# Kernel tuning notes

Measured on AMD Instinct MI355X. Metric: run time of the kernel, lower is better.

The kernel has to match this reference:

```python
import jax, jax.numpy as jnp
import numpy as np

HEADS = 4
NEG_SLOPE = 0.2
LN_EPS = 1e-5


def _layernorm(h, g, b):
    mu = h.mean(-1, keepdims=True)
    var = ((h - mu) ** 2).mean(-1, keepdims=True)
    return (h - mu) / jnp.sqrt(var + LN_EPS) * g + b


def _forward(x, edge_attr, vnf_context,
             w_node, b_node, w_edge_emb, b_edge_emb,
             w_eproj, b_eproj, w_vnf, b_vnf,
             attn_w1, attn_b1, attn_w2, attn_b2, attn_w3, attn_b3,
             gat_w, gat_att_src, gat_att_dst, gat_we, gat_att_e, gat_b,
             ln_g, ln_b,
             venc_w1, venc_b1, venc_w2, venc_b2,
             lstm_wih, lstm_whh, lstm_bih, lstm_bhh,
             out_w1, out_b1, out_w2, out_b2, out_w3, out_b3,
             edge_index):
    N = x.shape[0]
    C = w_node.shape[1]  # hidden_dim = per-head out_channels
    L = gat_w.shape[0]
    src, dst = edge_index[0], edge_index[1]

    # embeddings
    xh = x @ w_node + b_node                        # [N, C]
    ea = edge_attr @ w_edge_emb + b_edge_emb        # [E, C]

    # EdgeAttentionLayer (vnf_context branch, no network_state)
    ef = ea @ w_eproj + b_eproj                     # [E, C]
    vemb = vnf_context @ w_vnf + b_vnf              # [C]
    comb = jnp.concatenate([ef, jnp.broadcast_to(vemb, ef.shape)], axis=-1)
    h1 = jax.nn.relu(comb @ attn_w1 + attn_b1)
    h2 = jax.nn.relu(h1 @ attn_w2 + attn_b2)
    edge_attention = jax.nn.sigmoid(h2 @ attn_w3 + attn_b3)[:, 0]   # [E]
    e_enh = ef * edge_attention[:, None]            # weighted edge features [E, C]

    # PathQualityAwareConv stack: GATConv(heads=4, concat=False, edge_dim=C)
    for l in range(L):
        xr = xh
        xs = (xh @ gat_w[l]).reshape(N, HEADS, C)               # [N, H, C]
        efeat = (e_enh @ gat_we[l]).reshape(-1, HEADS, C)        # [E, H, C]
        a = (jnp.einsum('ehc,hc->eh', xs[src], gat_att_src[l])
             + jnp.einsum('ehc,hc->eh', xs[dst], gat_att_dst[l])
             + jnp.einsum('ehc,hc->eh', efeat, gat_att_e[l]))
        a = jax.nn.leaky_relu(a, NEG_SLOPE)
        amax = jax.ops.segment_max(a, dst, num_segments=N)
        amax = jnp.where(jnp.isfinite(amax), amax, 0.0)
        ae = jnp.exp(a - amax[dst])
        denom = jax.ops.segment_sum(ae, dst, num_segments=N)
        alpha = ae / (denom[dst] + 1e-16)                        # [E, H]
        msg = xs[src] * alpha[:, :, None]                        # [E, H, C]
        agg = jax.ops.segment_sum(msg, dst, num_segments=N)      # [N, H, C]
        h = agg.mean(axis=1) + gat_b[l]                          # concat=False -> head mean
        h = _layernorm(h, ln_g[l], ln_b[l])
        xh = h + xr                                              # residual (same size)

    # vnf context encoder
    v = jax.nn.relu(vnf_context @ venc_w1 + venc_b1) @ venc_w2 + venc_b2  # [C]

    # Set2Set pooling, single graph, processing_steps=3, LSTM(2C -> C)
    hS = jnp.zeros((C,), xh.dtype)
    cS = jnp.zeros((C,), xh.dtype)
    q_star = jnp.zeros((2 * C,), xh.dtype)
    for _ in range(3):
        gates = lstm_wih @ q_star + lstm_bih + lstm_whh @ hS + lstm_bhh
        gi, gf, gg, go = jnp.split(gates, 4)
        cS = jax.nn.sigmoid(gf) * cS + jax.nn.sigmoid(gi) * jnp.tanh(gg)
        hS = jax.nn.sigmoid(go) * jnp.tanh(cS)
        q = hS
        a_sc = jax.nn.softmax(xh @ q)                            # [N]
        r = a_sc @ xh                                            # [C]
        q_star = jnp.concatenate([q, r])

    combined = jnp.concatenate([q_star, v])                      # [3C]
    o = jax.nn.relu(combined @ out_w1 + out_b1)
    o = jax.nn.relu(o @ out_w2 + out_b2)
    o = jax.nn.relu(o @ out_w3 + out_b3)
    return o[None, :]                                            # [1, output_dim]


def setup_inputs() -> dict:
    key = jax.random.key(0)
    ks = jax.random.split(key, 40)
    N, E, C, L = 50000, 200000, 128, 3
    H = HEADS
    rn = lambda k, s, sc=0.05: (jax.random.normal(k, s, jnp.float32) * sc)
    z = lambda *s: jnp.zeros(s, jnp.float32)
    return {
        'x': jax.random.normal(ks[0], (N, 8), jnp.float32),
        'edge_index': jax.random.randint(ks[1], (2, E), 0, N),
        'edge_attr': jax.random.uniform(ks[2], (E, 4), dtype=jnp.float32),
        'vnf_context': jax.random.normal(ks[3], (6,), jnp.float32),
        'w_node': rn(ks[4], (8, C)), 'b_node': z(C),
        'w_edge_emb': rn(ks[5], (4, C)), 'b_edge_emb': z(C),
        'w_eproj': rn(ks[6], (C, C)), 'b_eproj': z(C),
        'w_vnf': rn(ks[7], (6, C)), 'b_vnf': z(C),
        'attn_w1': rn(ks[8], (2 * C, C)), 'attn_b1': z(C),
        'attn_w2': rn(ks[9], (C, C // 2)), 'attn_b2': z(C // 2),
        'attn_w3': rn(ks[10], (C // 2, 1)), 'attn_b3': z(1),
        'gat_w': rn(ks[11], (L, C, H * C)),
        'gat_att_src': rn(ks[12], (L, H, C)),
        'gat_att_dst': rn(ks[13], (L, H, C)),
        'gat_we': rn(ks[14], (L, C, H * C)),
        'gat_att_e': rn(ks[15], (L, H, C)),
        'gat_b': z(L, C),
        'ln_g': jnp.ones((L, C), jnp.float32), 'ln_b': z(L, C),
        'venc_w1': rn(ks[16], (6, C)), 'venc_b1': z(C),
        'venc_w2': rn(ks[17], (C, C)), 'venc_b2': z(C),
        'lstm_wih': rn(ks[18], (4 * C, 2 * C)), 'lstm_whh': rn(ks[19], (4 * C, C)),
        'lstm_bih': z(4 * C), 'lstm_bhh': z(4 * C),
        'out_w1': rn(ks[20], (3 * C, C)), 'out_b1': z(C),
        'out_w2': rn(ks[21], (C, C // 2)), 'out_b2': z(C // 2),
        'out_w3': rn(ks[22], (C // 2, 256)), 'out_b3': z(256),
    }


def reference(x, edge_index, edge_attr, vnf_context,
              w_node, b_node, w_edge_emb, b_edge_emb,
              w_eproj, b_eproj, w_vnf, b_vnf,
              attn_w1, attn_b1, attn_w2, attn_b2, attn_w3, attn_b3,
              gat_w, gat_att_src, gat_att_dst, gat_we, gat_att_e, gat_b,
              ln_g, ln_b,
              venc_w1, venc_b1, venc_w2, venc_b2,
              lstm_wih, lstm_whh, lstm_bih, lstm_bhh,
              out_w1, out_b1, out_w2, out_b2, out_w3, out_b3):
    return _forward(x, edge_attr, vnf_context,
                    w_node, b_node, w_edge_emb, b_edge_emb,
                    w_eproj, b_eproj, w_vnf, b_vnf,
                    attn_w1, attn_b1, attn_w2, attn_b2, attn_w3, attn_b3,
                    gat_w, gat_att_src, gat_att_dst, gat_we, gat_att_e, gat_b,
                    ln_g, ln_b,
                    venc_w1, venc_b1, venc_w2, venc_b2,
                    lstm_wih, lstm_whh, lstm_bih, lstm_bhh,
                    out_w1, out_b1, out_w2, out_b2, out_w3, out_b3,
                    edge_index)
```

## Files before the change

kernel.cpp:

```cpp
#include <hip/hip_runtime.h>
#include <math.h>

#define CC 128
#define HH 4
#define LL 3
#define LNEPS 1e-5f

typedef unsigned int u32;
typedef unsigned short ushort;
typedef float f32x16 __attribute__((ext_vector_type(16)));
typedef __bf16 bf16x8 __attribute__((ext_vector_type(8)));
union Frag { uint4 q; bf16x8 b; };

__device__ __forceinline__ u32 fenc(float f){ u32 u=__float_as_uint(f); return (u&0x80000000u)? ~u : (u|0x80000000u); }
__device__ __forceinline__ float fdec(u32 u){ return (u&0x80000000u)? __uint_as_float(u&0x7FFFFFFFu) : __uint_as_float(~u); }
__device__ __forceinline__ ushort bf16rne(float x){ u32 u=__float_as_uint(x); return (ushort)((u + 0x7FFF + ((u>>16)&1))>>16); }
__device__ __forceinline__ float bf2f(ushort h){ return __uint_as_float(((u32)h)<<16); }


__global__ void k_att_collapse(const float* __restrict__ W, const float* __restrict__ att, float* __restrict__ out){
  int idx = blockIdx.x*blockDim.x + threadIdx.x;
  if(idx >= LL*CC*HH) return;
  int h = idx % HH; int k = (idx/HH)%CC; int l = idx/(HH*CC);
  const float* w = W + ((size_t)(l*CC+k))*(HH*CC) + h*CC;
  const float* a = att + (size_t)(l*HH+h)*CC;
  float s=0.f;
  for(int c=0;c<CC;c++) s += w[c]*a[c];
  out[idx] = s;
}

__global__ void k_We(const float* __restrict__ w_ee, const float* __restrict__ w_ep, float* __restrict__ We){
  int idx = blockIdx.x*blockDim.x + threadIdx.x;
  if(idx >= 4*CC) return;
  int c = idx & (CC-1); int k = idx >> 7;
  float s=0.f;
  for(int m=0;m<CC;m++) s += w_ee[k*CC+m]*w_ep[m*CC+c];
  We[idx]=s;
}

__global__ void k_be_vemb(const float* __restrict__ b_ee, const float* __restrict__ w_ep, const float* __restrict__ b_ep,
                          const float* __restrict__ vnf, const float* __restrict__ w_vnf, const float* __restrict__ b_vnf,
                          float* __restrict__ be, float* __restrict__ vemb){
  int t = threadIdx.x;
  if(t<CC){
    float s=b_ep[t];
    for(int m=0;m<CC;m++) s += b_ee[m]*w_ep[m*CC+t];
    be[t]=s;
  } else if(t<2*CC){
    int c=t-CC;
    float s=b_vnf[c];
    for(int j=0;j<6;j++) s += vnf[j]*w_vnf[j*CC+c];
    vemb[c]=s;
  }
}

__global__ void k_h1eff(const float* __restrict__ We, const float* __restrict__ be, const float* __restrict__ vemb,
                        const float* __restrict__ w1, const float* __restrict__ b1,
                        float* __restrict__ Wh1, float* __restrict__ bh1){
  int idx = blockIdx.x*blockDim.x + threadIdx.x;
  if(idx < 4*CC){
    int c = idx & (CC-1); int k = idx>>7;
    float s=0.f;
    for(int m=0;m<CC;m++) s += We[k*CC+m]*w1[m*CC+c];
    Wh1[idx]=s;
  } else if(idx < 5*CC){
    int c = idx - 4*CC;
    float s=b1[c];
    for(int m=0;m<CC;m++) s += be[m]*w1[m*CC+c];
    for(int j=0;j<CC;j++) s += vemb[j]*w1[(CC+j)*CC+c];
    bh1[c]=s;
  }
}

__global__ void k_aelin(const float* __restrict__ We, const float* __restrict__ be, const float* __restrict__ wattE,
                        float* __restrict__ aelin, float* __restrict__ aebias){
  int t = threadIdx.x;
  if(t<48){
    int l=t>>4, k=(t>>2)&3, h=t&3;
    float s=0.f;
    for(int m=0;m<CC;m++) s += We[k*CC+m]*wattE[(size_t)(l*CC+m)*HH+h];
    aelin[t]=s;
  } else if(t<60){
    int i=t-48; int l=i>>2, h=i&3;
    float s=0.f;
    for(int m=0;m<CC;m++) s += be[m]*wattE[(size_t)(l*CC+m)*HH+h];
    aebias[i]=s;
  }
}

__global__ void k_wsplit(const float* __restrict__ gat_w, ushort* __restrict__ BHT, ushort* __restrict__ BLT){
  int idx = blockIdx.x*blockDim.x + threadIdx.x;
  if(idx >= LL*512*CC) return;
  int l = idx >> 16;
  int r = idx & 65535;
  int hk = r >> 7;
  int c  = r & 127;
  int k = hk & 127, h = hk >> 7;
  float v = gat_w[((size_t)(l*CC + k))*(HH*CC) + h*CC + c] * 0.25f;
  ushort hi = bf16rne(v);
  ushort lo = bf16rne(v - bf2f(hi));
  size_t pos = (size_t)l*65536 + ((size_t)(c>>5)*64 + (hk>>3))*256 + (size_t)((c&31)*8 + (hk&7));
  BHT[pos]=hi; BLT[pos]=lo;
}

__global__ void k_vvec(const float* __restrict__ vnf, const float* __restrict__ w1, const float* __restrict__ b1,
                       const float* __restrict__ w2, const float* __restrict__ b2, float* __restrict__ v){
  __shared__ float hv[CC];
  int t=threadIdx.x;
  float s=b1[t];
  for(int j=0;j<6;j++) s += vnf[j]*w1[j*CC+t];
  hv[t]=fmaxf(s,0.f);
  __syncthreads();
  float o=b2[t];
  for(int j=0;j<CC;j++) o += hv[j]*w2[j*CC+t];
  v[t]=o;
}

__global__ void k_node_embed(const float* __restrict__ x, const float* __restrict__ w, const float* __restrict__ b,
                             float* __restrict__ xh, int N){
  int idx=blockIdx.x*blockDim.x+threadIdx.x;
  if(idx>=N*CC) return;
  int c=idx&(CC-1); int n=idx>>7;
  const float* xr = x+(size_t)n*8;
  float s=b[c];
  #pragma unroll
  for(int k=0;k<8;k++) s += xr[k]*w[k*CC+c];
  xh[idx]=s;
}

__global__ void k_count(const int* __restrict__ dst, int* __restrict__ counts, int E){
  int e=blockIdx.x*blockDim.x+threadIdx.x;
  if(e<E) atomicAdd(&counts[dst[e]],1);
}

__global__ __launch_bounds__(256) void k_scan_blk(const int* __restrict__ counts, int* __restrict__ offsets,
                                                  int* __restrict__ bsum, int N){
  __shared__ int sv[256];
  int t=threadIdx.x; int i=blockIdx.x*256+t;
  int v = (i<N)? counts[i] : 0;
  sv[t]=v;
  __syncthreads();
  for(int off=1;off<256;off<<=1){
    int add = (t>=off)? sv[t-off]:0;
    __syncthreads();
    sv[t]+=add;
    __syncthreads();
  }
  if(i<N) offsets[i]=sv[t]-v;
  if(t==255) bsum[blockIdx.x]=sv[255];
}

__global__ __launch_bounds__(1024) void k_scan_top(int* __restrict__ bsum, int nb){
  __shared__ int sv[1024];
  int t=threadIdx.x;
  int v = (t<nb)? bsum[t] : 0;
  sv[t]=v;
  __syncthreads();
  for(int off=1;off<1024;off<<=1){
    int add = (t>=off)? sv[t-off]:0;
    __syncthreads();
    sv[t]+=add;
    __syncthreads();
  }
  if(t<nb) bsum[t]=sv[t]-v;
}

__global__ void k_scan_add(int* __restrict__ offsets, const int* __restrict__ bsum, int N, int E){
  int i=blockIdx.x*blockDim.x+threadIdx.x;
  if(i<N) offsets[i]+=bsum[i>>8];
  if(i==0) offsets[N]=E;
}

__global__ void k_fill(const int* __restrict__ dst, const int* __restrict__ offsets, int* __restrict__ cursor,
                       int* __restrict__ elist, int E){
  int e=blockIdx.x*blockDim.x+threadIdx.x;
  if(e<E){ int d=dst[e]; int pos=atomicAdd(&cursor[d],1); elist[offsets[d]+pos]=e; }
}

__global__ __launch_bounds__(256) void k_edge_attn(
    const float* __restrict__ edge_attr,
    const float* __restrict__ Wh1, const float* __restrict__ bh1,
    const float* __restrict__ attn_w2, const float* __restrict__ attn_b2,
    const float* __restrict__ attn_w3, const float* __restrict__ attn_b3,
    const float* __restrict__ aelin, const float* __restrict__ aebias,
    float* __restrict__ a_e, int E)
{
  __shared__ float s_w2[CC*64];
  __shared__ float s_h1t[64*64];
  __shared__ float s_eat[4*64];
  __shared__ float s_wh1t[CC*4];
  __shared__ float s_bh1[CC];
  __shared__ float s_b2[64];
  __shared__ float s_w3[64];
  __shared__ float s_lin[48];
  __shared__ float s_lbias[12];
  int t = threadIdx.x;
  for(int i=t;i<CC*64;i+=256) s_w2[i]=attn_w2[i];
  for(int i=t;i<CC*4;i+=256){ int c=i>>2, k=i&3; s_wh1t[i]=Wh1[k*CC+c]; }
  if(t<CC) s_bh1[t]=bh1[t];
  else if(t<CC+64) s_b2[t-CC]=attn_b2[t-CC];
  else if(t<CC+128) s_w3[t-CC-64]=attn_w3[t-CC-64];
  if(t<48) s_lin[t]=aelin[t];
  else if(t<60) s_lbias[t-48]=aebias[t-48];
  float b3v = attn_b3[0];
  int e0 = blockIdx.x*64;
  if(t<64){
    int e=e0+t;
    float4 v = (e<E)? *(const float4*)&edge_attr[(size_t)e*4] : make_float4(0.f,0.f,0.f,0.f);
    s_eat[t]=v.x; s_eat[64+t]=v.y; s_eat[128+t]=v.z; s_eat[192+t]=v.w;
  }
  int eg=t>>4, og=t&15;
  float acc[4][4];
  #pragma unroll
  for(int i=0;i<4;i++){ acc[i][0]=0.f; acc[i][1]=0.f; acc[i][2]=0.f; acc[i][3]=0.f; }
  for(int half=0;half<2;half++){
    __syncthreads();
    for(int i=t;i<64*64;i+=256){
      int kl=i>>6, e=i&63, k=half*64+kl;
      float4 w = *(const float4*)&s_wh1t[k*4];
      float v = s_bh1[k] + s_eat[e]*w.x + s_eat[64+e]*w.y + s_eat[128+e]*w.z + s_eat[192+e]*w.w;
      s_h1t[i] = fmaxf(v,0.f);
    }
    __syncthreads();
    const float* w2h = s_w2 + half*4096;
    #pragma unroll 8
    for(int k=0;k<64;k++){
      float4 a = *(const float4*)&s_h1t[k*64 + eg*4];
      float4 b = *(const float4*)&w2h[k*64 + og*4];
      acc[0][0]+=a.x*b.x; acc[0][1]+=a.x*b.y; acc[0][2]+=a.x*b.z; acc[0][3]+=a.x*b.w;
      acc[1][0]+=a.y*b.x; acc[1][1]+=a.y*b.y; acc[1][2]+=a.y*b.z; acc[1][3]+=a.y*b.w;
      acc[2][0]+=a.z*b.x; acc[2][1]+=a.z*b.y; acc[2][2]+=a.z*b.z; acc[2][3]+=a.z*b.w;
      acc[3][0]+=a.w*b.x; acc[3][1]+=a.w*b.y; acc[3][2]+=a.w*b.z; acc[3][3]+=a.w*b.w;
    }
  }
  float4 b2v = *(const float4*)&s_b2[og*4];
  float4 w3v = *(const float4*)&s_w3[og*4];
  float att[4];
  #pragma unroll
  for(int i=0;i<4;i++){
    float p = fmaxf(acc[i][0]+b2v.x,0.f)*w3v.x + fmaxf(acc[i][1]+b2v.y,0.f)*w3v.y
            + fmaxf(acc[i][2]+b2v.z,0.f)*w3v.z + fmaxf(acc[i][3]+b2v.w,0.f)*w3v.w;
    #pragma unroll
    for(int off=1;off<16;off<<=1) p += __shfl_xor(p,off);
    att[i] = 1.f/(1.f+expf(-(p+b3v)));
  }
  if(og<12){
    int l=og>>2, h=og&3;
    float w0=s_lin[l*16+h], w1=s_lin[l*16+4+h], w2x=s_lin[l*16+8+h], w3x=s_lin[l*16+12+h];
    float lb=s_lbias[l*4+h];
    #pragma unroll
    for(int i=0;i<4;i++){
      int el=eg*4+i; int e=e0+el;
      if(e<E){
        float v = s_eat[el]*w0 + s_eat[64+el]*w1 + s_eat[128+el]*w2x + s_eat[192+el]*w3x + lb;
        a_e[((size_t)l*E+e)*4+h] = att[i]*v;
      }
    }
  }
}

__global__ void k_node_ad(const float* __restrict__ xh, const float* __restrict__ wS, const float* __restrict__ wD,
                          float* __restrict__ asrc, float* __restrict__ adst, int N){
  int idx = blockIdx.x*blockDim.x + threadIdx.x;
  if(idx >= N*8) return;
  int o = idx & 7; int n = idx >> 3;
  const float* w = ((o<4)? wS : wD) + (o&3);
  const float* xr = xh + (size_t)n*CC;
  float s=0.f;
  for(int k=0;k<CC;k++) s += xr[k]*w[(size_t)k*HH];
  ((o<4)? asrc : adst)[n*4+(o&3)] = s;
}

__global__ __launch_bounds__(256) void k_aggregate(
    const float* __restrict__ xh, const int* __restrict__ srcArr,
    const float* __restrict__ aeL, const float* __restrict__ asrc, const float* __restrict__ adst,
    const int* __restrict__ offsets, const int* __restrict__ elist,
    ushort* __restrict__ sH, ushort* __restrict__ sL, int N)
{
  int wave = threadIdx.x>>6, lane = threadIdx.x&63;
  int n = blockIdx.x*4+wave;
  if(n>=N) return;
  int beg = offsets[n];
  int deg = offsets[n+1]-beg;
  const float4* ae4 = (const float4*)aeL;
  const float4* as4 = (const float4*)asrc;
  float4 ad = ((const float4*)adst)[n];
  float mx0=-1e30f,mx1=-1e30f,mx2=-1e30f,mx3=-1e30f;
  for(int base=0;base<deg;base+=64){
    int i=base+lane;
    if(i<deg){
      int e = elist[beg+i];
      float4 ae = ae4[e];
      float4 as = as4[srcArr[e]];
      float a0=as.x+ad.x+ae.x; a0=(a0>0.f)?a0:0.2f*a0;
      float a1=as.y+ad.y+ae.y; a1=(a1>0.f)?a1:0.2f*a1;
      float a2=as.z+ad.z+ae.z; a2=(a2>0.f)?a2:0.2f*a2;
      float a3=as.w+ad.w+ae.w; a3=(a3>0.f)?a3:0.2f*a3;
      mx0=fmaxf(mx0,a0); mx1=fmaxf(mx1,a1); mx2=fmaxf(mx2,a2); mx3=fmaxf(mx3,a3);
    }
  }
  #pragma unroll
  for(int o=32;o>=1;o>>=1){
    mx0=fmaxf(mx0,__shfl_xor(mx0,o));
    mx1=fmaxf(mx1,__shfl_xor(mx1,o));
    mx2=fmaxf(mx2,__shfl_xor(mx2,o));
    mx3=fmaxf(mx3,__shfl_xor(mx3,o));
  }
  float sm0=0,sm1=0,sm2=0,sm3=0;
  float acc0=0,acc1=0,acc2=0,acc3=0,acc4=0,acc5=0,acc6=0,acc7=0;
  for(int base=0;base<deg;base+=64){
    int i=base+lane;
    float ex0=0,ex1=0,ex2=0,ex3=0; int mysrc=0;
    if(i<deg){
      int e = elist[beg+i];
      mysrc = srcArr[e];
      float4 ae = ae4[e];
      float4 as = as4[mysrc];
      float a0=as.x+ad.x+ae.x; a0=(a0>0.f)?a0:0.2f*a0;
      float a1=as.y+ad.y+ae.y; a1=(a1>0.f)?a1:0.2f*a1;
      float a2=as.z+ad.z+ae.z; a2=(a2>0.f)?a2:0.2f*a2;
      float a3=as.w+ad.w+ae.w; a3=(a3>0.f)?a3:0.2f*a3;
      ex0=expf(a0-mx0); ex1=expf(a1-mx1); ex2=expf(a2-mx2); ex3=expf(a3-mx3);
      sm0+=ex0; sm1+=ex1; sm2+=ex2; sm3+=ex3;
    }
    int cnt = deg-base; if(cnt>64) cnt=64;
    for(int j=0;j<cnt;j++){
      int sr = __shfl(mysrc,j);
      float al0=__shfl(ex0,j), al1=__shfl(ex1,j), al2=__shfl(ex2,j), al3=__shfl(ex3,j);
      const float* xr = xh + (size_t)sr*CC;
      float x0 = xr[lane], x1 = xr[lane+64];
      acc0 += al0*x0; acc1 += al0*x1;
      acc2 += al1*x0; acc3 += al1*x1;
      acc4 += al2*x0; acc5 += al2*x1;
      acc6 += al3*x0; acc7 += al3*x1;
    }
  }
  #pragma unroll
  for(int o=32;o>=1;o>>=1){
    sm0+=__shfl_xor(sm0,o); sm1+=__shfl_xor(sm1,o); sm2+=__shfl_xor(sm2,o); sm3+=__shfl_xor(sm3,o);
  }
  float i0=1.f/(sm0+1e-16f), i1=1.f/(sm1+1e-16f), i2=1.f/(sm2+1e-16f), i3=1.f/(sm3+1e-16f);
  size_t rowbase = ((size_t)(n>>5))*64*256 + (size_t)((n&31)*8);
  auto put=[&](int hk, float v){
    ushort hi = bf16rne(v);
    ushort lo = bf16rne(v - bf2f(hi));
    size_t pos = rowbase + (size_t)(hk>>3)*256 + (hk&7);
    sH[pos]=hi; sL[pos]=lo;
  };
  put(lane, acc0*i0);      put(lane+64, acc1*i0);
  put(128+lane, acc2*i1);  put(128+lane+64, acc3*i1);
  put(256+lane, acc4*i2);  put(256+lane+64, acc5*i2);
  put(384+lane, acc6*i3);  put(384+lane+64, acc7*i3);
}

__global__ __launch_bounds__(128) void k_gemm_ln_mfma(
    const ushort* __restrict__ AH, const ushort* __restrict__ AL,
    const ushort* __restrict__ BH, const ushort* __restrict__ BL,
    const float* __restrict__ bias, const float* __restrict__ lng, const float* __restrict__ lnb,
    float* __restrict__ xh, int N)
{
  int tid = threadIdx.x;
  int w = tid>>6, lane = tid&63;
  int rlane = lane&31, khalf = lane>>5;
  int rb0 = blockIdx.x*4 + w*2;
  f32x16 acc[2][4];
  #pragma unroll
  for(int b=0;b<2;b++)
    #pragma unroll
    for(int t=0;t<4;t++)
      #pragma unroll
      for(int j=0;j<16;j++) acc[b][t][j]=0.f;

  const size_t laneoff = (size_t)(rlane*8);
  for(int ks=0; ks<32; ++ks){
    int kq = ks*2 + khalf;
    Frag ah[2], al[2];
    #pragma unroll
    for(int b=0;b<2;b++){
      size_t base = (((size_t)(rb0+b)*64 + kq)<<8) + laneoff;
      ah[b].q = *(const uint4*)(AH + base);
      al[b].q = *(const uint4*)(AL + base);
    }
    #pragma unroll
    for(int t=0;t<4;t++){
      size_t bb = (((size_t)t*64 + kq)<<8) + laneoff;
      Frag bh, bl;
      bh.q = *(const uint4*)(BH + bb);
      bl.q = *(const uint4*)(BL + bb);
      #pragma unroll
      for(int b=0;b<2;b++){
        acc[b][t] = __builtin_amdgcn_mfma_f32_32x32x16_bf16(ah[b].b, bh.b, acc[b][t], 0,0,0);
        acc[b][t] = __builtin_amdgcn_mfma_f32_32x32x16_bf16(ah[b].b, bl.b, acc[b][t], 0,0,0);
        acc[b][t] = __builtin_amdgcn_mfma_f32_32x32x16_bf16(al[b].b, bh.b, acc[b][t], 0,0,0);
      }
    }
  }
  float bias4[4], g4[4], eb4[4];
  #pragma unroll
  for(int t=0;t<4;t++){ int c=t*32+rlane; bias4[t]=bias[c]; g4[t]=lng[c]; eb4[t]=lnb[c]; }
  #pragma unroll
  for(int b=0;b<2;b++){
    #pragma unroll
    for(int reg=0; reg<16; ++reg){
      int rloc = (reg&3) + 8*(reg>>2) + 4*khalf;
      int grow = (rb0+b)*32 + rloc;
      float x0=acc[b][0][reg]+bias4[0];
      float x1=acc[b][1][reg]+bias4[1];
      float x2=acc[b][2][reg]+bias4[2];
      float x3=acc[b][3][reg]+bias4[3];
      float s = x0+x1+x2+x3;
      #pragma unroll
      for(int off=1; off<32; off<<=1) s += __shfl_xor(s, off);
      float mu = s*(1.f/CC);
      x0-=mu; x1-=mu; x2-=mu; x3-=mu;
      float q = x0*x0+x1*x1+x2*x2+x3*x3;
      #pragma unroll
      for(int off=1; off<32; off<<=1) q += __shfl_xor(q, off);
      float inv = rsqrtf(q*(1.f/CC)+LNEPS);
      if(grow < N){
        size_t gi = (size_t)grow*CC + rlane;
        xh[gi+ 0]  = x0*inv*g4[0] + eb4[0] + xh[gi+ 0];
        xh[gi+32]  = x1*inv*g4[1] + eb4[1] + xh[gi+32];
        xh[gi+64]  = x2*inv*g4[2] + eb4[2] + xh[gi+64];
        xh[gi+96]  = x3*inv*g4[3] + eb4[3] + xh[gi+96];
      }
    }
  }
}

__global__ __launch_bounds__(512) void k_lstm(const float* __restrict__ wih, const float* __restrict__ whh,
                    const float* __restrict__ bih, const float* __restrict__ bhh,
                    const float* __restrict__ qstar, float* __restrict__ hS, float* __restrict__ cS){
  __shared__ float sq[2*CC];
  __shared__ float sh[CC];
  __shared__ float sg[4*CC];
  int t=threadIdx.x;
  if(t<2*CC) sq[t]=qstar[t];
  else if(t<3*CC) sh[t-2*CC]=hS[t-2*CC];
  __syncthreads();
  float a=bih[t]+bhh[t];
  const float* wr = wih + (size_t)t*2*CC;
  for(int j=0;j<2*CC;j++) a += wr[j]*sq[j];
  const float* hr = whh + (size_t)t*CC;
  for(int j=0;j<CC;j++) a += hr[j]*sh[j];
  sg[t]=a;
  __syncthreads();
  if(t<CC){
    float gi=sg[t], gf=sg[CC+t], gg=sg[2*CC+t], go=sg[3*CC+t];
    float c = 1.f/(1.f+expf(-gf))*cS[t] + 1.f/(1.f+expf(-gi))*tanhf(gg);
    float h = 1.f/(1.f+expf(-go))*tanhf(c);
    cS[t]=c; hS[t]=h;
  }
}

__global__ __launch_bounds__(256) void k_scores(const float* __restrict__ xh, const float* __restrict__ q,
                                                float* __restrict__ sc, u32* __restrict__ scmax, int N){
  int t=threadIdx.x; int wave=t>>6, lane=t&63;
  float q0=q[lane], q1=q[lane+64];
  float wmax=-1e30f;
  for(int n=blockIdx.x*4+wave; n<N; n+=gridDim.x*4){
    const float* xr = xh+(size_t)n*CC;
    float v = xr[lane]*q0 + xr[lane+64]*q1;
    #pragma unroll
    for(int o=32;o>=1;o>>=1) v += __shfl_xor(v,o);
    if(lane==0) sc[n]=v;
    wmax = fmaxf(wmax,v);
  }
  __shared__ float sm[4];
  if(lane==0) sm[wave]=wmax;
  __syncthreads();
  if(t==0){
    float m = fmaxf(fmaxf(sm[0],sm[1]),fmaxf(sm[2],sm[3]));
    atomicMax(scmax, fenc(m));
  }
}

__global__ __launch_bounds__(256) void k_r(const float* __restrict__ xh, const float* __restrict__ sc,
                                           const u32* __restrict__ scmax, float* __restrict__ r,
                                           float* __restrict__ total, int N){
  int t=threadIdx.x; int c = t&(CC-1); int half = t>>7;
  float mx = fdec(*scmax);
  float acc=0.f, et=0.f;
  for(int n=blockIdx.x*2+half; n<N; n+=gridDim.x*2){
    float e = expf(sc[n]-mx);
    acc += e*xh[(size_t)n*CC+c];
    et += (c==0)? e : 0.f;
  }
  __shared__ float sacc[256];
  __shared__ float set_[2];
  sacc[t]=acc;
  if(c==0) set_[half]=et;
  __syncthreads();
  if(t<CC) atomicAdd(&r[t], sacc[t]+sacc[t+CC]);
  if(t==0) atomicAdd(total, set_[0]+set_[1]);
}

__global__ void k_finalize(const float* __restrict__ hS, const float* __restrict__ r,
                           const float* __restrict__ total, float* __restrict__ qstar){
  int t=threadIdx.x;
  if(t<CC) qstar[t]=hS[t];
  else if(t<2*CC) qstar[t]=r[t-CC]/total[0];
}

__global__ __launch_bounds__(256) void k_out(
  const float* __restrict__ qstar, const float* __restrict__ vvec,
  const float* __restrict__ w1, const float* __restrict__ b1,
  const float* __restrict__ w2, const float* __restrict__ b2,
  const float* __restrict__ w3, const float* __restrict__ b3, float* __restrict__ out)
{
  __shared__ float comb[3*CC];
  __shared__ float o1[CC];
  __shared__ float o2[64];
  int t=threadIdx.x;
  if(t<2*CC) comb[t]=qstar[t];
  if(t<CC) comb[2*CC+t]=vvec[t];
  __syncthreads();
  if(t<CC){
    float a=b1[t];
    for(int j=0;j<3*CC;j++) a += comb[j]*w1[j*CC+t];
    o1[t]=fmaxf(a,0.f);
  }
  __syncthreads();
  if(t<64){
    float a=b2[t];
    for(int j=0;j<CC;j++) a += o1[j]*w2[j*64+t];
    o2[t]=fmaxf(a,0.f);
  }
  __syncthreads();
  {
    float a=b3[t];
    for(int j=0;j<64;j++) a += o2[j]*w3[j*256+t];
    out[t]=fmaxf(a,0.f);
  }
}

extern "C" void kernel_launch(void* const* d_in, const int* in_sizes, int n_in,
                              void* d_out, int out_size, void* d_ws, size_t ws_size,
                              hipStream_t stream){
  (void)n_in; (void)out_size; (void)ws_size;
  const float* x        = (const float*)d_in[0];
  const int*   eidx     = (const int*)  d_in[1];
  const float* edge_attr= (const float*)d_in[2];
  const float* vnf      = (const float*)d_in[3];
  const float* w_node   = (const float*)d_in[4];
  const float* b_node   = (const float*)d_in[5];
  const float* w_ee     = (const float*)d_in[6];
  const float* b_ee     = (const float*)d_in[7];
  const float* w_ep     = (const float*)d_in[8];
  const float* b_ep     = (const float*)d_in[9];
  const float* w_vnf    = (const float*)d_in[10];
  const float* b_vnf    = (const float*)d_in[11];
  const float* attn_w1  = (const float*)d_in[12];
  const float* attn_b1  = (const float*)d_in[13];
  const float* attn_w2  = (const float*)d_in[14];
  const float* attn_b2  = (const float*)d_in[15];
  const float* attn_w3  = (const float*)d_in[16];
  const float* attn_b3  = (const float*)d_in[17];
  const float* gat_w    = (const float*)d_in[18];
  const float* att_src  = (const float*)d_in[19];
  const float* att_dst  = (const float*)d_in[20];
  const float* gat_we   = (const float*)d_in[21];
  const float* att_e    = (const float*)d_in[22];
  const float* gat_b    = (const float*)d_in[23];
  const float* ln_g     = (const float*)d_in[24];
  const float* ln_b     = (const float*)d_in[25];
  const float* venc_w1  = (const float*)d_in[26];
  const float* venc_b1  = (const float*)d_in[27];
  const float* venc_w2  = (const float*)d_in[28];
  const float* venc_b2  = (const float*)d_in[29];
  const float* lstm_wih = (const float*)d_in[30];
  const float* lstm_whh = (const float*)d_in[31];
  const float* lstm_bih = (const float*)d_in[32];
  const float* lstm_bhh = (const float*)d_in[33];
  const float* out_w1   = (const float*)d_in[34];
  const float* out_b1   = (const float*)d_in[35];
  const float* out_w2   = (const float*)d_in[36];
  const float* out_b2   = (const float*)d_in[37];
  const float* out_w3   = (const float*)d_in[38];
  const float* out_b3   = (const float*)d_in[39];

  const int N = in_sizes[0]/8;
  const int E = in_sizes[1]/2;
  const int* srcA = eidx;
  const int* dstA = eidx + E;

  const int Npad = ((N+127)/128)*128;
  const size_t atile = (size_t)(Npad/32)*64*256;
  const int nb = (N+255)/256;

  char* wp = (char*)d_ws;
  auto alloc = [&](size_t bytes)->void*{ void* p=(void*)wp; wp += (bytes+255)&~(size_t)255; return p; };
  float* xh    = (float*)alloc((size_t)N*CC*4);
  ushort* sbufH= (ushort*)alloc(atile*2);
  ushort* sbufL= (ushort*)alloc(atile*2);
  ushort* BHT  = (ushort*)alloc((size_t)LL*512*CC*2);
  ushort* BLT  = (ushort*)alloc((size_t)LL*512*CC*2);
  float* a_e   = (float*)alloc((size_t)LL*E*HH*4);
  float* asrc  = (float*)alloc((size_t)N*HH*4);
  float* adst  = (float*)alloc((size_t)N*HH*4);
  int* counts  = (int*)alloc((size_t)N*4);
  int* offsets = (int*)alloc((size_t)(N+1)*4);
  int* cursor  = (int*)alloc((size_t)N*4);
  int* elist   = (int*)alloc((size_t)E*4);
  int* bsum    = (int*)alloc((size_t)nb*4);
  float* sc    = (float*)alloc((size_t)N*4);
  float* wattS = (float*)alloc((size_t)LL*CC*HH*4);
  float* wattD = (float*)alloc((size_t)LL*CC*HH*4);
  float* wattE = (float*)alloc((size_t)LL*CC*HH*4);
  float* We    = (float*)alloc(4*CC*4);
  float* be    = (float*)alloc(CC*4);
  float* vemb  = (float*)alloc(CC*4);
  float* Wh1   = (float*)alloc(4*CC*4);
  float* bh1   = (float*)alloc(CC*4);
  float* aelin = (float*)alloc(48*4);
  float* aebias= (float*)alloc(12*4);
  float* vvec  = (float*)alloc(CC*4);
  float* lbuf  = (float*)alloc(4*CC*4);
  float* hS=lbuf; float* cS=lbuf+CC; float* qstar=lbuf+2*CC;
  float* s2s   = (float*)alloc(130*4);

  k_att_collapse<<<6,256,0,stream>>>(gat_w, att_src, wattS);
  k_att_collapse<<<6,256,0,stream>>>(gat_w, att_dst, wattD);
  k_att_collapse<<<6,256,0,stream>>>(gat_we, att_e, wattE);
  k_We<<<2,256,0,stream>>>(w_ee, w_ep, We);
  k_be_vemb<<<1,256,0,stream>>>(b_ee, w_ep, b_ep, vnf, w_vnf, b_vnf, be, vemb);
  k_h1eff<<<3,256,0,stream>>>(We, be, vemb, attn_w1, attn_b1, Wh1, bh1);
  k_aelin<<<1,64,0,stream>>>(We, be, wattE, aelin, aebias);
  k_wsplit<<<(LL*512*CC+255)/256,256,0,stream>>>(gat_w, BHT, BLT);
  k_vvec<<<1,CC,0,stream>>>(vnf, venc_w1, venc_b1, venc_w2, venc_b2, vvec);
  k_node_embed<<<(N*CC+255)/256,256,0,stream>>>(x, w_node, b_node, xh, N);

  hipMemsetAsync(counts, 0, (size_t)N*4, stream);
  k_count<<<(E+255)/256,256,0,stream>>>(dstA, counts, E);
  k_scan_blk<<<nb,256,0,stream>>>(counts, offsets, bsum, N);
  k_scan_top<<<1,1024,0,stream>>>(bsum, nb);
  k_scan_add<<<nb,256,0,stream>>>(offsets, bsum, N, E);
  hipMemsetAsync(cursor, 0, (size_t)N*4, stream);
  k_fill<<<(E+255)/256,256,0,stream>>>(dstA, offsets, cursor, elist, E);

  k_edge_attn<<<(E+63)/64,256,0,stream>>>(edge_attr, Wh1, bh1, attn_w2, attn_b2, attn_w3, attn_b3, aelin, aebias, a_e, E);

  for(int l=0;l<LL;l++){
    k_node_ad<<<(N*8+255)/256,256,0,stream>>>(xh, wattS+(size_t)l*CC*HH, wattD+(size_t)l*CC*HH, asrc, adst, N);
    k_aggregate<<<(N+3)/4,256,0,stream>>>(xh, srcA, a_e+(size_t)l*E*HH, asrc, adst, offsets, elist, sbufH, sbufL, N);
    k_gemm_ln_mfma<<<Npad/128,128,0,stream>>>(sbufH, sbufL,
                                              BHT+(size_t)l*512*CC, BLT+(size_t)l*512*CC,
                                              gat_b+(size_t)l*CC, ln_g+(size_t)l*CC, ln_b+(size_t)l*CC, xh, N);
  }

  hipMemsetAsync(lbuf, 0, 4*CC*4, stream);
  for(int it=0; it<3; ++it){
    k_lstm<<<1,512,0,stream>>>(lstm_wih, lstm_whh, lstm_bih, lstm_bhh, qstar, hS, cS);
    hipMemsetAsync(s2s, 0, 130*4, stream);
    k_scores<<<512,256,0,stream>>>(xh, hS, sc, (u32*)s2s, N);
    k_r<<<512,256,0,stream>>>(xh, sc, (u32*)s2s, s2s+2, s2s+1, N);
    k_finalize<<<1,256,0,stream>>>(hS, s2s+2, s2s+1, qstar);
  }

  k_out<<<1,256,0,stream>>>(qstar, vvec, out_w1, out_b1, out_w2, out_b2, out_w3, out_b3, (float*)d_out);
}
```

Before: 836.8 us.

## Restructure GAT softmax, node projections, GEMM tiling and Set2Set pooling kernels

Splits the per-node edge softmax into a separate per-(node,head) alpha kernel that writes normalized weights in place, and simplifies aggregation to a single pass with float2 loads and packed bf16 stores. It also tiles k_node_ad through shared memory and halves the per-wave row blocks in the MFMA GEMM so more blocks launch. Set2Set pooling becomes a single-pass online-softmax kernel with per-block partials plus a small reduce, dropping the memsets, atomics and score buffer. Edge-attention stages W2 in halves to cut shared memory. The alpha kernel walks edges serially per thread, which may be slow for high-degree nodes.

```diff
diff --git a/kernel.cpp b/kernel.cpp
--- a/kernel.cpp
+++ b/kernel.cpp
@@ -12,8 +12,6 @@
 typedef __bf16 bf16x8 __attribute__((ext_vector_type(8)));
 union Frag { uint4 q; bf16x8 b; };
 
-__device__ __forceinline__ u32 fenc(float f){ u32 u=__float_as_uint(f); return (u&0x80000000u)? ~u : (u|0x80000000u); }
-__device__ __forceinline__ float fdec(u32 u){ return (u&0x80000000u)? __uint_as_float(u&0x7FFFFFFFu) : __uint_as_float(~u); }
 __device__ __forceinline__ ushort bf16rne(float x){ u32 u=__float_as_uint(x); return (ushort)((u + 0x7FFF + ((u>>16)&1))>>16); }
 __device__ __forceinline__ float bf2f(ushort h){ return __uint_as_float(((u32)h)<<16); }
 
@@ -185,7 +183,7 @@
     const float* __restrict__ aelin, const float* __restrict__ aebias,
     float* __restrict__ a_e, int E)
 {
-  __shared__ float s_w2[CC*64];
+  __shared__ float s_w2[64*64];
   __shared__ float s_h1t[64*64];
   __shared__ float s_eat[4*64];
   __shared__ float s_wh1t[CC*4];
@@ -195,7 +193,6 @@
   __shared__ float s_lin[48];
   __shared__ float s_lbias[12];
   int t = threadIdx.x;
-  for(int i=t;i<CC*64;i+=256) s_w2[i]=attn_w2[i];
   for(int i=t;i<CC*4;i+=256){ int c=i>>2, k=i&3; s_wh1t[i]=Wh1[k*CC+c]; }
   if(t<CC) s_bh1[t]=bh1[t];
   else if(t<CC+64) s_b2[t-CC]=attn_b2[t-CC];
@@ -221,12 +218,12 @@
       float v = s_bh1[k] + s_eat[e]*w.x + s_eat[64+e]*w.y + s_eat[128+e]*w.z + s_eat[192+e]*w.w;
       s_h1t[i] = fmaxf(v,0.f);
     }
+    for(int i=t;i<64*64;i+=256) s_w2[i] = attn_w2[half*4096 + i];
     __syncthreads();
-    const float* w2h = s_w2 + half*4096;
     #pragma unroll 8
     for(int k=0;k<64;k++){
       float4 a = *(const float4*)&s_h1t[k*64 + eg*4];
-      float4 b = *(const float4*)&w2h[k*64 + og*4];
+      float4 b = *(const float4*)&s_w2[k*64 + og*4];
       acc[0][0]+=a.x*b.x; acc[0][1]+=a.x*b.y; acc[0][2]+=a.x*b.z; acc[0][3]+=a.x*b.w;
       acc[1][0]+=a.y*b.x; acc[1][1]+=a.y*b.y; acc[1][2]+=a.y*b.z; acc[1][3]+=a.y*b.w;
       acc[2][0]+=a.z*b.x; acc[2][1]+=a.z*b.y; acc[2][2]+=a.z*b.z; acc[2][3]+=a.z*b.w;
@@ -259,98 +256,92 @@
   }
 }
 
-__global__ void k_node_ad(const float* __restrict__ xh, const float* __restrict__ wS, const float* __restrict__ wD,
+__global__ __launch_bounds__(256) void k_node_ad(const float* __restrict__ xh, const float* __restrict__ wS, const float* __restrict__ wD,
                           float* __restrict__ asrc, float* __restrict__ adst, int N){
+  __shared__ float sx[32*129];
+  __shared__ float sw[CC*8];
+  int t = threadIdx.x;
+  int n0 = blockIdx.x*32;
+  for(int i=t;i<512;i+=256){ int k=i>>2, h=i&3; sw[k*8+h]=wS[i]; sw[k*8+4+h]=wD[i]; }
+  int lim = (N-n0 < 32 ? N-n0 : 32)*128;
+  for(int i=t;i<lim;i+=256){ int nl=i>>7, k=i&127; sx[nl*129+k] = xh[(size_t)n0*128 + i]; }
+  __syncthreads();
+  int node = t>>3, o = t&7;
+  if(n0+node < N){
+    const float* xr = sx + node*129;
+    float s=0.f;
+    #pragma unroll 8
+    for(int k=0;k<CC;k++) s += xr[k]*sw[k*8+o];
+    ((o<4)? asrc : adst)[(n0+node)*4 + (o&3)] = s;
+  }
+}
+
+__global__ void k_alpha(const float* __restrict__ asrc, const float* __restrict__ adst,
+                        const int* __restrict__ offsets, const int* __restrict__ elist,
+                        const int* __restrict__ srcArr, float* __restrict__ ael, int N){
   int idx = blockIdx.x*blockDim.x + threadIdx.x;
-  if(idx >= N*8) return;
-  int o = idx & 7; int n = idx >> 3;
-  const float* w = ((o<4)? wS : wD) + (o&3);
-  const float* xr = xh + (size_t)n*CC;
+  if(idx >= N*4) return;
+  int n = idx>>2, h = idx&3;
+  int beg = offsets[n], end = offsets[n+1];
+  if(beg==end) return;
+  float ad = adst[n*4+h];
+  float m = -1e30f;
+  for(int i=beg;i<end;i++){
+    int e = elist[i];
+    float a = asrc[srcArr[e]*4+h] + ad + ael[e*4+h];
+    a = (a>0.f)? a : 0.2f*a;
+    m = fmaxf(m,a);
+  }
   float s=0.f;
-  for(int k=0;k<CC;k++) s += xr[k]*w[(size_t)k*HH];
-  ((o<4)? asrc : adst)[n*4+(o&3)] = s;
+  for(int i=beg;i<end;i++){
+    int e = elist[i];
+    float a = asrc[srcArr[e]*4+h] + ad + ael[e*4+h];
+    a = (a>0.f)? a : 0.2f*a;
+    float ex = expf(a-m);
+    s += ex;
+    ael[e*4+h] = ex;
+  }
+  float inv = 1.f/(s+1e-16f);
+  for(int i=beg;i<end;i++){
+    int e = elist[i];
+    ael[e*4+h] *= inv;
+  }
 }
 
 __global__ __launch_bounds__(256) void k_aggregate(
     const float* __restrict__ xh, const int* __restrict__ srcArr,
-    const float* __restrict__ aeL, const float* __restrict__ asrc, const float* __restrict__ adst,
-    const int* __restrict__ offsets, const int* __restrict__ elist,
+    const float* __restrict__ alpha, const int* __restrict__ offsets, const int* __restrict__ elist,
     ushort* __restrict__ sH, ushort* __restrict__ sL, int N)
 {
   int wave = threadIdx.x>>6, lane = threadIdx.x&63;
   int n = blockIdx.x*4+wave;
   if(n>=N) return;
-  int beg = offsets[n];
-  int deg = offsets[n+1]-beg;
-  const float4* ae4 = (const float4*)aeL;
-  const float4* as4 = (const float4*)asrc;
-  float4 ad = ((const float4*)adst)[n];
-  float mx0=-1e30f,mx1=-1e30f,mx2=-1e30f,mx3=-1e30f;
-  for(int base=0;base<deg;base+=64){
-    int i=base+lane;
-    if(i<deg){
-      int e = elist[beg+i];
-      float4 ae = ae4[e];
-      float4 as = as4[srcArr[e]];
-      float a0=as.x+ad.x+ae.x; a0=(a0>0.f)?a0:0.2f*a0;
-      float a1=as.y+ad.y+ae.y; a1=(a1>0.f)?a1:0.2f*a1;
-      float a2=as.z+ad.z+ae.z; a2=(a2>0.f)?a2:0.2f*a2;
-      float a3=as.w+ad.w+ae.w; a3=(a3>0.f)?a3:0.2f*a3;
-      mx0=fmaxf(mx0,a0); mx1=fmaxf(mx1,a1); mx2=fmaxf(mx2,a2); mx3=fmaxf(mx3,a3);
-    }
-  }
-  #pragma unroll
-  for(int o=32;o>=1;o>>=1){
-    mx0=fmaxf(mx0,__shfl_xor(mx0,o));
-    mx1=fmaxf(mx1,__shfl_xor(mx1,o));
-    mx2=fmaxf(mx2,__shfl_xor(mx2,o));
-    mx3=fmaxf(mx3,__shfl_xor(mx3,o));
-  }
-  float sm0=0,sm1=0,sm2=0,sm3=0;
-  float acc0=0,acc1=0,acc2=0,acc3=0,acc4=0,acc5=0,acc6=0,acc7=0;
-  for(int base=0;base<deg;base+=64){
-    int i=base+lane;
-    float ex0=0,ex1=0,ex2=0,ex3=0; int mysrc=0;
-    if(i<deg){
-      int e = elist[beg+i];
-      mysrc = srcArr[e];
-      float4 ae = ae4[e];
-      float4 as = as4[mysrc];
-      float a0=as.x+ad.x+ae.x; a0=(a0>0.f)?a0:0.2f*a0;
-      float a1=as.y+ad.y+ae.y; a1=(a1>0.f)?a1:0.2f*a1;
-      float a2=as.z+ad.z+ae.z; a2=(a2>0.f)?a2:0.2f*a2;
-      float a3=as.w+ad.w+ae.w; a3=(a3>0.f)?a3:0.2f*a3;
-      ex0=expf(a0-mx0); ex1=expf(a1-mx1); ex2=expf(a2-mx2); ex3=expf(a3-mx3);
-      sm0+=ex0; sm1+=ex1; sm2+=ex2; sm3+=ex3;
-    }
-    int cnt = deg-base; if(cnt>64) cnt=64;
-    for(int j=0;j<cnt;j++){
-      int sr = __shfl(mysrc,j);
-      float al0=__shfl(ex0,j), al1=__shfl(ex1,j), al2=__shfl(ex2,j), al3=__shfl(ex3,j);
-      const float* xr = xh + (size_t)sr*CC;
-      float x0 = xr[lane], x1 = xr[lane+64];
-      acc0 += al0*x0; acc1 += al0*x1;
-      acc2 += al1*x0; acc3 += al1*x1;
-      acc4 += al2*x0; acc5 += al2*x1;
-      acc6 += al3*x0; acc7 += al3*x1;
-    }
-  }
-  #pragma unroll
-  for(int o=32;o>=1;o>>=1){
-    sm0+=__shfl_xor(sm0,o); sm1+=__shfl_xor(sm1,o); sm2+=__shfl_xor(sm2,o); sm3+=__shfl_xor(sm3,o);
-  }
-  float i0=1.f/(sm0+1e-16f), i1=1.f/(sm1+1e-16f), i2=1.f/(sm2+1e-16f), i3=1.f/(sm3+1e-16f);
-  size_t rowbase = ((size_t)(n>>5))*64*256 + (size_t)((n&31)*8);
-  auto put=[&](int hk, float v){
-    ushort hi = bf16rne(v);
-    ushort lo = bf16rne(v - bf2f(hi));
+  int beg = offsets[n], end = offsets[n+1];
+  const float4* al4 = (const float4*)alpha;
+  float2 ac[4];
+  #pragma unroll
+  for(int h=0;h<4;h++){ ac[h].x=0.f; ac[h].y=0.f; }
+  for(int i=beg;i<end;i++){
+    int e = elist[i];
+    int sr = srcArr[e];
+    float4 a = al4[e];
+    float2 x = *(const float2*)&xh[(size_t)sr*CC + lane*2];
+    ac[0].x += a.x*x.x; ac[0].y += a.x*x.y;
+    ac[1].x += a.y*x.x; ac[1].y += a.y*x.y;
+    ac[2].x += a.z*x.x; ac[2].y += a.z*x.y;
+    ac[3].x += a.w*x.x; ac[3].y += a.w*x.y;
+  }
+  size_t rowbase = ((size_t)(n>>5))*16384 + (size_t)((n&31)*8);
+  #pragma unroll
+  for(int h=0;h<4;h++){
+    ushort h0 = bf16rne(ac[h].x), h1 = bf16rne(ac[h].y);
+    u32 hi = (u32)h0 | ((u32)h1<<16);
+    u32 lo = (u32)bf16rne(ac[h].x - bf2f(h0)) | ((u32)bf16rne(ac[h].y - bf2f(h1))<<16);
+    int hk = h*CC + lane*2;
     size_t pos = rowbase + (size_t)(hk>>3)*256 + (hk&7);
-    sH[pos]=hi; sL[pos]=lo;
-  };
-  put(lane, acc0*i0);      put(lane+64, acc1*i0);
-  put(128+lane, acc2*i1);  put(128+lane+64, acc3*i1);
-  put(256+lane, acc4*i2);  put(256+lane+64, acc5*i2);
-  put(384+lane, acc6*i3);  put(384+lane+64, acc7*i3);
+    *(u32*)&sH[pos] = hi;
+    *(u32*)&sL[pos] = lo;
+  }
 }
 
 __global__ __launch_bounds__(128) void k_gemm_ln_mfma(
@@ -362,68 +353,57 @@
   int tid = threadIdx.x;
   int w = tid>>6, lane = tid&63;
   int rlane = lane&31, khalf = lane>>5;
-  int rb0 = blockIdx.x*4 + w*2;
-  f32x16 acc[2][4];
-  #pragma unroll
-  for(int b=0;b<2;b++)
+  int rb = blockIdx.x*2 + w;
+  f32x16 acc[4];
+  #pragma unroll
+  for(int t=0;t<4;t++)
     #pragma unroll
-    for(int t=0;t<4;t++)
-      #pragma unroll
-      for(int j=0;j<16;j++) acc[b][t][j]=0.f;
+    for(int j=0;j<16;j++) acc[t][j]=0.f;
 
   const size_t laneoff = (size_t)(rlane*8);
   for(int ks=0; ks<32; ++ks){
     int kq = ks*2 + khalf;
-    Frag ah[2], al[2];
-    #pragma unroll
-    for(int b=0;b<2;b++){
-      size_t base = (((size_t)(rb0+b)*64 + kq)<<8) + laneoff;
-      ah[b].q = *(const uint4*)(AH + base);
-      al[b].q = *(const uint4*)(AL + base);
-    }
+    size_t base = (((size_t)rb*64 + kq)<<8) + laneoff;
+    Frag ah, al;
+    ah.q = *(const uint4*)(AH + base);
+    al.q = *(const uint4*)(AL + base);
     #pragma unroll
     for(int t=0;t<4;t++){
       size_t bb = (((size_t)t*64 + kq)<<8) + laneoff;
       Frag bh, bl;
       bh.q = *(const uint4*)(BH + bb);
       bl.q = *(const uint4*)(BL + bb);
-      #pragma unroll
-      for(int b=0;b<2;b++){
-        acc[b][t] = __builtin_amdgcn_mfma_f32_32x32x16_bf16(ah[b].b, bh.b, acc[b][t], 0,0,0);
-        acc[b][t] = __builtin_amdgcn_mfma_f32_32x32x16_bf16(ah[b].b, bl.b, acc[b][t], 0,0,0);
-        acc[b][t] = __builtin_amdgcn_mfma_f32_32x32x16_bf16(al[b].b, bh.b, acc[b][t], 0,0,0);
-      }
+      acc[t] = __builtin_amdgcn_mfma_f32_32x32x16_bf16(ah.b, bh.b, acc[t], 0,0,0);
+      acc[t] = __builtin_amdgcn_mfma_f32_32x32x16_bf16(ah.b, bl.b, acc[t], 0,0,0);
+      acc[t] = __builtin_amdgcn_mfma_f32_32x32x16_bf16(al.b, bh.b, acc[t], 0,0,0);
     }
   }
   float bias4[4], g4[4], eb4[4];
   #pragma unroll
   for(int t=0;t<4;t++){ int c=t*32+rlane; bias4[t]=bias[c]; g4[t]=lng[c]; eb4[t]=lnb[c]; }
   #pragma unroll
-  for(int b=0;b<2;b++){
+  for(int reg=0; reg<16; ++reg){
+    int rloc = (reg&3) + 8*(reg>>2) + 4*khalf;
+    int grow = rb*32 + rloc;
+    float x0=acc[0][reg]+bias4[0];
+    float x1=acc[1][reg]+bias4[1];
+    float x2=acc[2][reg]+bias4[2];
+    float x3=acc[3][reg]+bias4[3];
+    float s = x0+x1+x2+x3;
     #pragma unroll
-    for(int reg=0; reg<16; ++reg){
-      int rloc = (reg&3) + 8*(reg>>2) + 4*khalf;
-      int grow = (rb0+b)*32 + rloc;
-      float x0=acc[b][0][reg]+bias4[0];
-      float x1=acc[b][1][reg]+bias4[1];
-      float x2=acc[b][2][reg]+bias4[2];
-      float x3=acc[b][3][reg]+bias4[3];
-      float s = x0+x1+x2+x3;
-      #pragma unroll
-      for(int off=1; off<32; off<<=1) s += __shfl_xor(s, off);
-      float mu = s*(1.f/CC);
-      x0-=mu; x1-=mu; x2-=mu; x3-=mu;
-      float q = x0*x0+x1*x1+x2*x2+x3*x3;
-      #pragma unroll
-      for(int off=1; off<32; off<<=1) q += __shfl_xor(q, off);
-      float inv = rsqrtf(q*(1.f/CC)+LNEPS);
-      if(grow < N){
-        size_t gi = (size_t)grow*CC + rlane;
-        xh[gi+ 0]  = x0*inv*g4[0] + eb4[0] + xh[gi+ 0];
-        xh[gi+32]  = x1*inv*g4[1] + eb4[1] + xh[gi+32];
-        xh[gi+64]  = x2*inv*g4[2] + eb4[2] + xh[gi+64];
-        xh[gi+96]  = x3*inv*g4[3] + eb4[3] + xh[gi+96];
-      }
+    for(int off=1; off<32; off<<=1) s += __shfl_xor(s, off);
+    float mu = s*(1.f/CC);
+    x0-=mu; x1-=mu; x2-=mu; x3-=mu;
+    float q = x0*x0+x1*x1+x2*x2+x3*x3;
+    #pragma unroll
+    for(int off=1; off<32; off<<=1) q += __shfl_xor(q, off);
+    float inv = rsqrtf(q*(1.f/CC)+LNEPS);
+    if(grow < N){
+      size_t gi = (size_t)grow*CC + rlane;
+      xh[gi+ 0]  = x0*inv*g4[0] + eb4[0] + xh[gi+ 0];
+      xh[gi+32]  = x1*inv*g4[1] + eb4[1] + xh[gi+32];
+      xh[gi+64]  = x2*inv*g4[2] + eb4[2] + xh[gi+64];
+      xh[gi+96]  = x3*inv*g4[3] + eb4[3] + xh[gi+96];
     }
   }
 }
@@ -453,53 +433,48 @@
   }
 }
 
-__global__ __launch_bounds__(256) void k_scores(const float* __restrict__ xh, const float* __restrict__ q,
-                                                float* __restrict__ sc, u32* __restrict__ scmax, int N){
-  int t=threadIdx.x; int wave=t>>6, lane=t&63;
+__global__ __launch_bounds__(256) void k_s2s1(const float* __restrict__ xh, const float* __restrict__ q,
+                                              float* __restrict__ pm, float* __restrict__ ps,
+                                              float* __restrict__ pr, int N){
+  int t=threadIdx.x, wave=t>>6, lane=t&63;
   float q0=q[lane], q1=q[lane+64];
-  float wmax=-1e30f;
+  float m=-1e30f, s=0.f, r0=0.f, r1=0.f;
   for(int n=blockIdx.x*4+wave; n<N; n+=gridDim.x*4){
     const float* xr = xh+(size_t)n*CC;
-    float v = xr[lane]*q0 + xr[lane+64]*q1;
+    float x0 = xr[lane], x1 = xr[lane+64];
+    float v = x0*q0 + x1*q1;
     #pragma unroll
     for(int o=32;o>=1;o>>=1) v += __shfl_xor(v,o);
-    if(lane==0) sc[n]=v;
-    wmax = fmaxf(wmax,v);
-  }
-  __shared__ float sm[4];
-  if(lane==0) sm[wave]=wmax;
-  __syncthreads();
-  if(t==0){
-    float m = fmaxf(fmaxf(sm[0],sm[1]),fmaxf(sm[2],sm[3]));
-    atomicMax(scmax, fenc(m));
-  }
-}
-
-__global__ __launch_bounds__(256) void k_r(const float* __restrict__ xh, const float* __restrict__ sc,
-                                           const u32* __restrict__ scmax, float* __restrict__ r,
-                                           float* __restrict__ total, int N){
-  int t=threadIdx.x; int c = t&(CC-1); int half = t>>7;
-  float mx = fdec(*scmax);
-  float acc=0.f, et=0.f;
-  for(int n=blockIdx.x*2+half; n<N; n+=gridDim.x*2){
-    float e = expf(sc[n]-mx);
-    acc += e*xh[(size_t)n*CC+c];
-    et += (c==0)? e : 0.f;
-  }
-  __shared__ float sacc[256];
-  __shared__ float set_[2];
-  sacc[t]=acc;
-  if(c==0) set_[half]=et;
-  __syncthreads();
-  if(t<CC) atomicAdd(&r[t], sacc[t]+sacc[t+CC]);
-  if(t==0) atomicAdd(total, set_[0]+set_[1]);
-}
-
-__global__ void k_finalize(const float* __restrict__ hS, const float* __restrict__ r,
-                           const float* __restrict__ total, float* __restrict__ qstar){
+    float nm = fmaxf(m,v);
+    float f = expf(m-nm), g = expf(v-nm);
+    s = s*f + g; r0 = r0*f + g*x0; r1 = r1*f + g*x1;
+    m = nm;
+  }
+  __shared__ float sm[4], ss[4], sr[4][128];
+  if(lane==0){ sm[wave]=m; ss[wave]=s; }
+  sr[wave][lane]=r0; sr[wave][lane+64]=r1;
+  __syncthreads();
+  if(t<128){
+    float M = fmaxf(fmaxf(sm[0],sm[1]),fmaxf(sm[2],sm[3]));
+    float e0=expf(sm[0]-M), e1=expf(sm[1]-M), e2=expf(sm[2]-M), e3=expf(sm[3]-M);
+    pr[(size_t)blockIdx.x*128+t] = sr[0][t]*e0 + sr[1][t]*e1 + sr[2][t]*e2 + sr[3][t]*e3;
+    if(t==0){ pm[blockIdx.x]=M; ps[blockIdx.x]= ss[0]*e0+ss[1]*e1+ss[2]*e2+ss[3]*e3; }
+  }
+}
+
+__global__ void k_s2s2(const float* __restrict__ pm, const float* __restrict__ ps, const float* __restrict__ pr,
+                       const float* __restrict__ hS, float* __restrict__ qstar, int NB){
   int t=threadIdx.x;
-  if(t<CC) qstar[t]=hS[t];
-  else if(t<2*CC) qstar[t]=r[t-CC]/total[0];
+  float M=-1e30f;
+  for(int b=0;b<NB;b++) M = fmaxf(M, pm[b]);
+  float rs=0.f, ssum=0.f;
+  for(int b=0;b<NB;b++){
+    float w = expf(pm[b]-M);
+    rs   += pr[(size_t)b*128+t]*w;
+    ssum += ps[b]*w;
+  }
+  qstar[t]     = hS[t];
+  qstar[CC+t]  = rs/ssum;
 }
 
 __global__ __launch_bounds__(256) void k_out(
@@ -587,6 +562,7 @@
   const int Npad = ((N+127)/128)*128;
   const size_t atile = (size_t)(Npad/32)*64*256;
   const int nb = (N+255)/256;
+  const int S2SB = 256;
 
   char* wp = (char*)d_ws;
   auto alloc = [&](size_t bytes)->void*{ void* p=(void*)wp; wp += (bytes+255)&~(size_t)255; return p; };
@@ -603,7 +579,6 @@
   int* cursor  = (int*)alloc((size_t)N*4);
   int* elist   = (int*)alloc((size_t)E*4);
   int* bsum    = (int*)alloc((size_t)nb*4);
-  float* sc    = (float*)alloc((size_t)N*4);
   float* wattS = (float*)alloc((size_t)LL*CC*HH*4);
   float* wattD = (float*)alloc((size_t)LL*CC*HH*4);
   float* wattE = (float*)alloc((size_t)LL*CC*HH*4);
@@ -617,7 +592,9 @@
   float* vvec  = (float*)alloc(CC*4);
   float* lbuf  = (float*)alloc(4*CC*4);
   float* hS=lbuf; float* cS=lbuf+CC; float* qstar=lbuf+2*CC;
-  float* s2s   = (float*)alloc(130*4);
+  float* pm    = (float*)alloc((size_t)S2SB*4);
+  float* ps    = (float*)alloc((size_t)S2SB*4);
+  float* pr    = (float*)alloc((size_t)S2SB*128*4);
 
   k_att_collapse<<<6,256,0,stream>>>(gat_w, att_src, wattS);
   k_att_collapse<<<6,256,0,stream>>>(gat_w, att_dst, wattD);
@@ -641,20 +618,20 @@
   k_edge_attn<<<(E+63)/64,256,0,stream>>>(edge_attr, Wh1, bh1, attn_w2, attn_b2, attn_w3, attn_b3, aelin, aebias, a_e, E);
 
   for(int l=0;l<LL;l++){
-    k_node_ad<<<(N*8+255)/256,256,0,stream>>>(xh, wattS+(size_t)l*CC*HH, wattD+(size_t)l*CC*HH, asrc, adst, N);
-    k_aggregate<<<(N+3)/4,256,0,stream>>>(xh, srcA, a_e+(size_t)l*E*HH, asrc, adst, offsets, elist, sbufH, sbufL, N);
-    k_gemm_ln_mfma<<<Npad/128,128,0,stream>>>(sbufH, sbufL,
-                                              BHT+(size_t)l*512*CC, BLT+(size_t)l*512*CC,
-                                              gat_b+(size_t)l*CC, ln_g+(size_t)l*CC, ln_b+(size_t)l*CC, xh, N);
+    float* ael = a_e + (size_t)l*E*HH;
+    k_node_ad<<<(N+31)/32,256,0,stream>>>(xh, wattS+(size_t)l*CC*HH, wattD+(size_t)l*CC*HH, asrc, adst, N);
+    k_alpha<<<(N*4+255)/256,256,0,stream>>>(asrc, adst, offsets, elist, srcA, ael, N);
+    k_aggregate<<<(N+3)/4,256,0,stream>>>(xh, srcA, ael, offsets, elist, sbufH, sbufL, N);
+    k_gemm_ln_mfma<<<Npad/64,128,0,stream>>>(sbufH, sbufL,
+                                             BHT+(size_t)l*512*CC, BLT+(size_t)l*512*CC,
+                                             gat_b+(size_t)l*CC, ln_g+(size_t)l*CC, ln_b+(size_t)l*CC, xh, N);
   }
 
   hipMemsetAsync(lbuf, 0, 4*CC*4, stream);
   for(int it=0; it<3; ++it){
     k_lstm<<<1,512,0,stream>>>(lstm_wih, lstm_whh, lstm_bih, lstm_bhh, qstar, hS, cS);
-    hipMemsetAsync(s2s, 0, 130*4, stream);
-    k_scores<<<512,256,0,stream>>>(xh, hS, sc, (u32*)s2s, N);
-    k_r<<<512,256,0,stream>>>(xh, sc, (u32*)s2s, s2s+2, s2s+1, N);
-    k_finalize<<<1,256,0,stream>>>(hS, s2s+2, s2s+1, qstar);
+    k_s2s1<<<S2SB,256,0,stream>>>(xh, hS, pm, ps, pr, N);
+    k_s2s2<<<1,128,0,stream>>>(pm, ps, pr, hS, qstar, S2SB);
   }
 
   k_out<<<1,256,0,stream>>>(qstar, vvec, out_w1, out_b1, out_w2, out_b2, out_w3, out_b3, (float*)d_out);
```

New measurement: 1.083 ms. 29.4% more time.
